# Kernel tuning notes

Hardware: AMD Instinct MI355X
Metric: run time of the kernel (lower is better)

Reference implementation:

```python
import jax, jax.numpy as jnp
import numpy as np

INV_SQRT2 = 0.7071067811865476  # Haar (db1) filter coefficient


def _haar_wavedec(x, level):
    """Haar (db1) multi-level DWT along axis=2 of x: [B,H,L,Dh].
    Returns [cA_n, cD_n, cD_{n-1}, ..., cD_1] (pywt.wavedec ordering).
    Exact match to pywt for L divisible by 2**level (no boundary padding needed)."""
    details = []
    a = x
    for _ in range(level):
        e, o = a[:, :, 0::2, :], a[:, :, 1::2, :]
        details.append((e - o) * INV_SQRT2)
        a = (e + o) * INV_SQRT2
    return [a] + details[::-1]


def _haar_idwt_step(a, d):
    """Single-level Haar inverse DWT along axis=2."""
    e = (a + d) * INV_SQRT2
    o = (a - d) * INV_SQRT2
    B, H, Lh, Dh = a.shape
    return jnp.stack([e, o], axis=3).reshape(B, H, 2 * Lh, Dh)


def setup_inputs() -> dict:
    key = jax.random.key(0)
    ks = jax.random.split(key, 6)
    B, L, D, H, M = 8, 4096, 1024, 16, 3
    Dh = D // H
    return {
        "query": jax.random.normal(ks[0], (B, L, D), jnp.float32),
        "W_qkv": jax.random.normal(ks[1], (3 * D, D), jnp.float32) * 0.02,
        "b_qkv": jnp.zeros((3 * D,), jnp.float32),
        "W_out": jax.random.normal(ks[2], (D, D), jnp.float32) * 0.02,
        "b_out": jnp.zeros((D,), jnp.float32),
        "weight_q": jax.random.normal(ks[3], (H, M, Dh), jnp.float32),
        "weight_v": jax.random.normal(ks[4], (H, M, Dh), jnp.float32),
    }


def reference(query, W_qkv, b_qkv, W_out, b_out, weight_q, weight_v):
    B, L, D = query.shape
    H, M, Dh = weight_q.shape  # n_heads, modes, head_dim

    qkv = query @ W_qkv.T + b_qkv               # [B,L,3D]; k chunk is unused (as in original)
    q = qkv[..., :D].reshape(B, L, H, Dh).transpose(0, 2, 1, 3)      # [B,H,L,Dh]
    v = qkv[..., 2 * D:].reshape(B, L, H, Dh).transpose(0, 2, 1, 3)  # [B,H,L,Dh]

    cq = _haar_wavedec(q, M)  # [cA_M, cD_M, ..., cD_1]
    cv = _haar_wavedec(v, M)

    # Weight the coarsest `modes` bands per head/channel, then multiply q*v in wavelet domain.
    prod = []
    for j in range(M):
        wq = weight_q[None, :, j, None, :]  # [1,H,1,Dh]
        wv = weight_v[None, :, j, None, :]
        prod.append((cq[j] * wq) * (cv[j] * wv))
    prod.append(cq[M] * cv[M])  # finest detail band, unweighted

    # Inverse DWT back to length L.
    a = prod[0]
    for d in prod[1:]:
        a = _haar_idwt_step(a, d)

    out = a.transpose(0, 2, 1, 3).reshape(B, L, D)
    return out @ W_out.T + b_out  # dropout is identity in eval
```

## Files before the change

### kernel.cpp

```cpp
#include <hip/hip_runtime.h>
#include <hip/hip_fp16.h>
#include <cstdint>
#include <cstddef>

typedef _Float16 f16;
typedef __attribute__((ext_vector_type(4))) _Float16 f16x4;
typedef __attribute__((ext_vector_type(8))) _Float16 f16x8;
typedef __attribute__((ext_vector_type(4))) float f32x4;

#define C_INV_SQRT2 0.70710678118654752440f

__device__ __forceinline__ void gld_lds16(const void* g, void* l) {
  __builtin_amdgcn_global_load_lds((const __attribute__((address_space(1))) void*)g,
                                   (__attribute__((address_space(3))) void*)l, 16, 0, 0);
}

__global__ __launch_bounds__(256) void cvt_f32_f16_k(const float* __restrict__ in,
                                                     f16* __restrict__ out, int n4) {
  int i = blockIdx.x * 256 + threadIdx.x;
  if (i >= n4) return;
  const float4 x = ((const float4*)in)[i];
  f16x4 y;
  y.x = (f16)x.x; y.y = (f16)x.y; y.z = (f16)x.z; y.w = (f16)x.w;
  ((f16x4*)out)[i] = y;
}

__global__ __launch_bounds__(256) void pack_wqv_k(const float* __restrict__ W,
                                                  const float* __restrict__ b,
                                                  f16* __restrict__ Wo,
                                                  float* __restrict__ bo) {
  int i = blockIdx.x * 256 + threadIdx.x;
  int n = i >> 8;
  int c = (i & 255) * 4;
  int sn = (n < 1024) ? n : (n + 1024);
  const float4 x = *(const float4*)(W + (size_t)sn * 1024 + c);
  f16x4 y; y.x = (f16)x.x; y.y = (f16)x.y; y.z = (f16)x.z; y.w = (f16)x.w;
  *(f16x4*)(Wo + (size_t)n * 1024 + c) = y;
  if (i < 2048) bo[i] = b[(i < 1024) ? i : (i + 1024)];
}


#define STAGEH(bufi, mat, half, k0)                                              \
  {                                                                              \
    f16* Ld = &lds[bufi][mat][half][0];                                          \
    const f16* Gp =                                                              \
        ((mat) ? GB : GA) + (size_t)((half) * 128 + srow) * K + (k0) + sch * 8;  \
    gld_lds16(Gp, Ld + (w * 64) * 8);                                            \
    gld_lds16(Gp + (size_t)64 * K, Ld + (4096 + w * 64 * 8));                    \
  }

#define MFMA_PH(mi0)                                                             \
  __builtin_amdgcn_s_setprio(1);                                                 \
  _Pragma("unroll") for (int mm = (mi0); mm < (mi0) + 2; mm++)                   \
      _Pragma("unroll") for (int nj = 0; nj < 4; nj++) {                         \
    acc[mm][nj] = __builtin_amdgcn_mfma_f32_16x16x32_f16(aF[mm][0], bF[nj][0],   \
                                                         acc[mm][nj], 0, 0, 0);  \
    acc[mm][nj] = __builtin_amdgcn_mfma_f32_16x16x32_f16(aF[mm][1], bF[nj][1],   \
                                                         acc[mm][nj], 0, 0, 0);  \
  }                                                                              \
  __builtin_amdgcn_s_setprio(0);

#define BAR_SEQ()                       \
  __builtin_amdgcn_sched_barrier(0);    \
  __builtin_amdgcn_s_barrier();         \
  __builtin_amdgcn_sched_barrier(0);

template <typename CT>
__global__ __launch_bounds__(512, 2) void gemm256_k(const f16* __restrict__ A,
                                                    const f16* __restrict__ B,
                                                    const float* __restrict__ bias,
                                                    CT* __restrict__ C,
                                                    int M, int N, int K, int nbx) {
  __shared__ f16 lds[2][2][2][128 * 64];
  const int t = threadIdx.x;
  const int w = t >> 6, l = t & 63;
  const int wm = w >> 2, wn = w & 3;
  const int hi = l >> 4, lo = l & 15;

  const int nwg = gridDim.x;
  const int cpx = nwg >> 3;
  const int bid = blockIdx.x;
  const int nid = (bid & 7) * cpx + (bid >> 3);
  const int by = nid / nbx, bx = nid - by * nbx;
  const int m0 = by * 256, n0 = bx * 256;

  const f16* GA = A + (size_t)m0 * K;
  const f16* GB = B + (size_t)n0 * K;

  const int srow = t >> 3;
  const int sch = (t & 7) ^ (srow & 7);

  const int colk0 = ((hi ^ (lo & 7)) << 3);
  const int colk1 = (((4 | hi) ^ (lo & 7)) << 3);

  f32x4 acc[8][4] = {};
  f16x8 aF[8][2], bF[4][2];
  const int NT = K >> 6;

  STAGEH(0, 0, 0, 0); STAGEH(0, 0, 1, 0);
  STAGEH(0, 1, 0, 0); STAGEH(0, 1, 1, 0);
  STAGEH(1, 0, 0, 64); STAGEH(1, 0, 1, 64);

  for (int tt = 0; tt < NT; ++tt) {
    const int buf = tt & 1;
    const f16* pA = &lds[buf][0][wm][0] + lo * 64;
    const f16* pB = &lds[buf][1][wn >> 1][0] + (wn & 1) * 4096 + lo * 64;
    const f16* pA0 = pA + colk0;
    const f16* pA1 = pA + colk1;
    const f16* pB0 = pB + colk0;
    const f16* pB1 = pB + colk1;

    if (tt < NT - 1) {
      asm volatile("s_waitcnt vmcnt(4)" ::: "memory");
    } else {
      asm volatile("s_waitcnt vmcnt(0)" ::: "memory");
    }
    BAR_SEQ();
    aF[0][0] = *(const f16x8*)(pA0 + 0 * 1024);
    aF[0][1] = *(const f16x8*)(pA1 + 0 * 1024);
    aF[1][0] = *(const f16x8*)(pA0 + 1 * 1024);
    aF[1][1] = *(const f16x8*)(pA1 + 1 * 1024);
#pragma unroll
    for (int nj = 0; nj < 4; nj++) {
      bF[nj][0] = *(const f16x8*)(pB0 + nj * 1024);
      bF[nj][1] = *(const f16x8*)(pB1 + nj * 1024);
    }
    aF[2][0] = *(const f16x8*)(pA0 + 2 * 1024);
    aF[2][1] = *(const f16x8*)(pA1 + 2 * 1024);
    aF[3][0] = *(const f16x8*)(pA0 + 3 * 1024);
    aF[3][1] = *(const f16x8*)(pA1 + 3 * 1024);
    if (tt + 1 < NT) STAGEH(buf ^ 1, 1, 0, (tt + 1) * 64);
    MFMA_PH(0);

    BAR_SEQ();
#pragma unroll
    for (int mi = 4; mi < 8; mi++) {
      aF[mi][0] = *(const f16x8*)(pA0 + mi * 1024);
      aF[mi][1] = *(const f16x8*)(pA1 + mi * 1024);
    }
    if (tt + 1 < NT) STAGEH(buf ^ 1, 1, 1, (tt + 1) * 64);
    MFMA_PH(2);

    asm volatile("s_waitcnt lgkmcnt(0)" ::: "memory");
    BAR_SEQ();
    if (tt + 2 < NT) STAGEH(buf, 0, 0, (tt + 2) * 64);
    MFMA_PH(4);

    asm volatile("s_waitcnt lgkmcnt(0)" ::: "memory");
    BAR_SEQ();
    if (tt + 2 < NT) STAGEH(buf, 0, 1, (tt + 2) * 64);
    MFMA_PH(6);
  }

#pragma unroll
  for (int mi = 0; mi < 8; mi++) {
#pragma unroll
    for (int nj = 0; nj < 4; nj++) {
      const int col = n0 + wn * 64 + nj * 16 + lo;
      const float bb = bias[col];
      const size_t base = (size_t)(m0 + wm * 128 + mi * 16 + hi * 4) * N + col;
#pragma unroll
      for (int r = 0; r < 4; r++) C[base + (size_t)r * N] = (CT)(acc[mi][nj][r] + bb);
    }
  }
}

__global__ __launch_bounds__(256) void dwt_middle_k(const f16* __restrict__ qv,
                                                    const float* __restrict__ wq,
                                                    const float* __restrict__ wv,
                                                    f16* __restrict__ out) {
  const int g = blockIdx.x;
  const int d0 = threadIdx.x * 4;
  const size_t m0 = (size_t)g * 8;

  f16x4 qr[8], vr[8], o[8];
#pragma unroll
  for (int i = 0; i < 8; i++) {
    qr[i] = *(const f16x4*)(qv + (m0 + i) * 2048 + d0);
    vr[i] = *(const f16x4*)(qv + (m0 + i) * 2048 + 1024 + d0);
  }
  const float c = C_INV_SQRT2;
#pragma unroll
  for (int dd = 0; dd < 4; dd++) {
    const int d = d0 + dd;
    const int h = d >> 6, dh = d & 63;
    float q[8], v[8];
#pragma unroll
    for (int i = 0; i < 8; i++) { q[i] = (float)qr[i][dd]; v[i] = (float)vr[i][dd]; }

    float qa1[4], qd1[4], va1[4], vd1[4];
#pragma unroll
    for (int i = 0; i < 4; i++) {
      qd1[i] = (q[2 * i] - q[2 * i + 1]) * c;
      qa1[i] = (q[2 * i] + q[2 * i + 1]) * c;
      vd1[i] = (v[2 * i] - v[2 * i + 1]) * c;
      va1[i] = (v[2 * i] + v[2 * i + 1]) * c;
    }
    float qa2[2], qd2[2], va2[2], vd2[2];
#pragma unroll
    for (int j = 0; j < 2; j++) {
      qd2[j] = (qa1[2 * j] - qa1[2 * j + 1]) * c;
      qa2[j] = (qa1[2 * j] + qa1[2 * j + 1]) * c;
      vd2[j] = (va1[2 * j] - va1[2 * j + 1]) * c;
      va2[j] = (va1[2 * j] + va1[2 * j + 1]) * c;
    }
    const float qd3 = (qa2[0] - qa2[1]) * c, qa3 = (qa2[0] + qa2[1]) * c;
    const float vd3 = (va2[0] - va2[1]) * c, va3 = (va2[0] + va2[1]) * c;

    const int wb = h * 192 + dh;
    const float wq0 = wq[wb], wq1 = wq[wb + 64], wq2 = wq[wb + 128];
    const float wv0 = wv[wb], wv1 = wv[wb + 64], wv2 = wv[wb + 128];

    const float pa = (qa3 * wq0) * (va3 * wv0);
    const float pd3 = (qd3 * wq1) * (vd3 * wv1);
    float pd2[2], pd1[4];
#pragma unroll
    for (int j = 0; j < 2; j++) pd2[j] = (qd2[j] * wq2) * (vd2[j] * wv2);
#pragma unroll
    for (int i = 0; i < 4; i++) pd1[i] = qd1[i] * vd1[i];

    float s2[2], s1[4];
    s2[0] = (pa + pd3) * c;
    s2[1] = (pa - pd3) * c;
#pragma unroll
    for (int j = 0; j < 2; j++) {
      s1[2 * j] = (s2[j] + pd2[j]) * c;
      s1[2 * j + 1] = (s2[j] - pd2[j]) * c;
    }
#pragma unroll
    for (int i = 0; i < 4; i++) {
      o[2 * i][dd] = (f16)((s1[i] + pd1[i]) * c);
      o[2 * i + 1][dd] = (f16)((s1[i] - pd1[i]) * c);
    }
  }
#pragma unroll
  for (int i = 0; i < 8; i++) *(f16x4*)(out + (m0 + i) * 1024 + d0) = o[i];
}

extern "C" void kernel_launch(void* const* d_in, const int* in_sizes, int n_in,
                              void* d_out, int out_size, void* d_ws, size_t ws_size,
                              hipStream_t stream) {
  (void)in_sizes; (void)n_in; (void)out_size; (void)ws_size;
  const float* query = (const float*)d_in[0];
  const float* W_qkv = (const float*)d_in[1];
  const float* b_qkv = (const float*)d_in[2];
  const float* W_out = (const float*)d_in[3];
  const float* b_out = (const float*)d_in[4];
  const float* wq = (const float*)d_in[5];
  const float* wv = (const float*)d_in[6];
  float* out = (float*)d_out;

  char* ws = (char*)d_ws;
  f16* qf16 = (f16*)ws;
  f16* Wqv = (f16*)(ws + 67108864);
  float* bqv = (float*)(ws + 67108864 + 4194304);
  f16* Wout = (f16*)(ws + 67108864 + 4194304 + 8192);
  f16* qv = (f16*)d_out;
  f16* a_f16 = qf16;

  cvt_f32_f16_k<<<dim3(8388608 / 256), dim3(256), 0, stream>>>(query, qf16, 8388608);
  pack_wqv_k<<<dim3(2048), dim3(256), 0, stream>>>(W_qkv, b_qkv, Wqv, bqv);
  cvt_f32_f16_k<<<dim3(262144 / 256), dim3(256), 0, stream>>>(W_out, Wout, 262144);
  gemm256_k<f16><<<dim3((2048 / 256) * (32768 / 256)), dim3(512), 0, stream>>>(
      qf16, Wqv, bqv, qv, 32768, 2048, 1024, 2048 / 256);
  dwt_middle_k<<<dim3(4096), dim3(256), 0, stream>>>(qv, wq, wv, a_f16);
  gemm256_k<float><<<dim3((1024 / 256) * (32768 / 256)), dim3(512), 0, stream>>>(
      a_f16, Wout, b_out, out, 32768, 1024, 1024, 1024 / 256);
}
```

Baseline: 286.1 us.

## Fuse Haar wavelet middle stage into QV projection GEMM epilogue

The QV projection GEMM now gives each block 128 q columns and the matching 128 v columns, so the Haar forward transform, band weighting, product and inverse transform can run in the epilogue. The accumulators are staged through swizzled LDS and written straight to the f16 activation buffer, which removes the separate dwt_middle kernel and the round trip of the 2048-wide qv intermediate through global memory. The fused path needs a larger workspace and falls back to the old three-kernel path when the workspace is too small. The epilogue adds LDS traffic, a barrier and scalar global stores with stride across rows.

```diff
diff --git a/kernel.cpp b/kernel.cpp
--- a/kernel.cpp
+++ b/kernel.cpp
@@ -39,14 +39,61 @@
   if (i < 2048) bo[i] = b[(i < 1024) ? i : (i + 1024)];
 }
 
-
-#define STAGEH(bufi, mat, half, k0)                                              \
-  {                                                                              \
-    f16* Ld = &lds[bufi][mat][half][0];                                          \
-    const f16* Gp =                                                              \
-        ((mat) ? GB : GA) + (size_t)((half) * 128 + srow) * K + (k0) + sch * 8;  \
-    gld_lds16(Gp, Ld + (w * 64) * 8);                                            \
-    gld_lds16(Gp + (size_t)64 * K, Ld + (4096 + w * 64 * 8));                    \
+__device__ __forceinline__ void haar_mid(const f16x8 q8, const f16x8 v8,
+                                         float wq0, float wq1, float wq2,
+                                         float wv0, float wv1, float wv2,
+                                         float* a8) {
+  const float c = C_INV_SQRT2;
+  float q[8], v[8];
+#pragma unroll
+  for (int i = 0; i < 8; i++) { q[i] = (float)q8[i]; v[i] = (float)v8[i]; }
+  float qa1[4], qd1[4], va1[4], vd1[4];
+#pragma unroll
+  for (int i = 0; i < 4; i++) {
+    qd1[i] = (q[2 * i] - q[2 * i + 1]) * c;
+    qa1[i] = (q[2 * i] + q[2 * i + 1]) * c;
+    vd1[i] = (v[2 * i] - v[2 * i + 1]) * c;
+    va1[i] = (v[2 * i] + v[2 * i + 1]) * c;
+  }
+  float qa2[2], qd2[2], va2[2], vd2[2];
+#pragma unroll
+  for (int j = 0; j < 2; j++) {
+    qd2[j] = (qa1[2 * j] - qa1[2 * j + 1]) * c;
+    qa2[j] = (qa1[2 * j] + qa1[2 * j + 1]) * c;
+    vd2[j] = (va1[2 * j] - va1[2 * j + 1]) * c;
+    va2[j] = (va1[2 * j] + va1[2 * j + 1]) * c;
+  }
+  const float qd3 = (qa2[0] - qa2[1]) * c, qa3 = (qa2[0] + qa2[1]) * c;
+  const float vd3 = (va2[0] - va2[1]) * c, va3 = (va2[0] + va2[1]) * c;
+  const float pa = (qa3 * wq0) * (va3 * wv0);
+  const float pd3 = (qd3 * wq1) * (vd3 * wv1);
+  float pd2[2], pd1[4];
+#pragma unroll
+  for (int j = 0; j < 2; j++) pd2[j] = (qd2[j] * wq2) * (vd2[j] * wv2);
+#pragma unroll
+  for (int i = 0; i < 4; i++) pd1[i] = qd1[i] * vd1[i];
+  float s2[2], s1[4];
+  s2[0] = (pa + pd3) * c;
+  s2[1] = (pa - pd3) * c;
+#pragma unroll
+  for (int j = 0; j < 2; j++) {
+    s1[2 * j] = (s2[j] + pd2[j]) * c;
+    s1[2 * j + 1] = (s2[j] - pd2[j]) * c;
+  }
+#pragma unroll
+  for (int i = 0; i < 4; i++) {
+    a8[2 * i] = (s1[i] + pd1[i]) * c;
+    a8[2 * i + 1] = (s1[i] - pd1[i]) * c;
+  }
+}
+
+
+#define STAGEH(bufi, mat, half, Gbase, k0)                         \
+  {                                                                \
+    f16* Ld = &lds[bufi][mat][half][0];                            \
+    const f16* Gp = (Gbase) + (size_t)srow * K + (k0) + sch * 8;   \
+    gld_lds16(Gp, Ld + (w * 64) * 8);                              \
+    gld_lds16(Gp + (size_t)64 * K, Ld + (4096 + w * 64 * 8));      \
   }
 
 #define MFMA_PH(mi0)                                                             \
@@ -65,11 +112,13 @@
   __builtin_amdgcn_s_barrier();         \
   __builtin_amdgcn_sched_barrier(0);
 
-template <typename CT>
+template <typename CT, bool FUSED>
 __global__ __launch_bounds__(512, 2) void gemm256_k(const f16* __restrict__ A,
                                                     const f16* __restrict__ B,
                                                     const float* __restrict__ bias,
                                                     CT* __restrict__ C,
+                                                    const float* __restrict__ wq,
+                                                    const float* __restrict__ wv,
                                                     int M, int N, int K, int nbx) {
   __shared__ f16 lds[2][2][2][128 * 64];
   const int t = threadIdx.x;
@@ -82,10 +131,13 @@
   const int bid = blockIdx.x;
   const int nid = (bid & 7) * cpx + (bid >> 3);
   const int by = nid / nbx, bx = nid - by * nbx;
-  const int m0 = by * 256, n0 = bx * 256;
+  const int m0 = by * 256;
+  const int n0 = bx * 256;
+  const int d0 = bx * 128;
 
   const f16* GA = A + (size_t)m0 * K;
-  const f16* GB = B + (size_t)n0 * K;
+  const f16* GBq = FUSED ? (B + (size_t)d0 * K) : (B + (size_t)n0 * K);
+  const f16* GBv = FUSED ? (B + (size_t)(1024 + d0) * K) : (GBq + (size_t)128 * K);
 
   const int srow = t >> 3;
   const int sch = (t & 7) ^ (srow & 7);
@@ -97,9 +149,9 @@
   f16x8 aF[8][2], bF[4][2];
   const int NT = K >> 6;
 
-  STAGEH(0, 0, 0, 0); STAGEH(0, 0, 1, 0);
-  STAGEH(0, 1, 0, 0); STAGEH(0, 1, 1, 0);
-  STAGEH(1, 0, 0, 64); STAGEH(1, 0, 1, 64);
+  STAGEH(0, 0, 0, GA, 0); STAGEH(0, 0, 1, GA + (size_t)128 * K, 0);
+  STAGEH(0, 1, 0, GBq, 0); STAGEH(0, 1, 1, GBv, 0);
+  STAGEH(1, 0, 0, GA, 64); STAGEH(1, 0, 1, GA + (size_t)128 * K, 64);
 
   for (int tt = 0; tt < NT; ++tt) {
     const int buf = tt & 1;
@@ -129,7 +181,7 @@
     aF[2][1] = *(const f16x8*)(pA1 + 2 * 1024);
     aF[3][0] = *(const f16x8*)(pA0 + 3 * 1024);
     aF[3][1] = *(const f16x8*)(pA1 + 3 * 1024);
-    if (tt + 1 < NT) STAGEH(buf ^ 1, 1, 0, (tt + 1) * 64);
+    if (tt + 1 < NT) STAGEH(buf ^ 1, 1, 0, GBq, (tt + 1) * 64);
     MFMA_PH(0);
 
     BAR_SEQ();
@@ -138,29 +190,66 @@
       aF[mi][0] = *(const f16x8*)(pA0 + mi * 1024);
       aF[mi][1] = *(const f16x8*)(pA1 + mi * 1024);
     }
-    if (tt + 1 < NT) STAGEH(buf ^ 1, 1, 1, (tt + 1) * 64);
+    if (tt + 1 < NT) STAGEH(buf ^ 1, 1, 1, GBv, (tt + 1) * 64);
     MFMA_PH(2);
 
     asm volatile("s_waitcnt lgkmcnt(0)" ::: "memory");
     BAR_SEQ();
-    if (tt + 2 < NT) STAGEH(buf, 0, 0, (tt + 2) * 64);
+    if (tt + 2 < NT) STAGEH(buf, 0, 0, GA, (tt + 2) * 64);
     MFMA_PH(4);
 
     asm volatile("s_waitcnt lgkmcnt(0)" ::: "memory");
     BAR_SEQ();
-    if (tt + 2 < NT) STAGEH(buf, 0, 1, (tt + 2) * 64);
+    if (tt + 2 < NT) STAGEH(buf, 0, 1, GA + (size_t)128 * K, (tt + 2) * 64);
     MFMA_PH(6);
   }
 
-#pragma unroll
-  for (int mi = 0; mi < 8; mi++) {
-#pragma unroll
-    for (int nj = 0; nj < 4; nj++) {
-      const int col = n0 + wn * 64 + nj * 16 + lo;
-      const float bb = bias[col];
-      const size_t base = (size_t)(m0 + wm * 128 + mi * 16 + hi * 4) * N + col;
-#pragma unroll
-      for (int r = 0; r < 4; r++) C[base + (size_t)r * N] = (CT)(acc[mi][nj][r] + bb);
+  if (!FUSED) {
+#pragma unroll
+    for (int mi = 0; mi < 8; mi++) {
+#pragma unroll
+      for (int nj = 0; nj < 4; nj++) {
+        const int col = n0 + wn * 64 + nj * 16 + lo;
+        const float bb = bias[col];
+        const size_t base = (size_t)(m0 + wm * 128 + mi * 16 + hi * 4) * N + col;
+#pragma unroll
+        for (int r = 0; r < 4; r++) C[base + (size_t)r * N] = (CT)(acc[mi][nj][r] + bb);
+      }
+    }
+  } else {
+    char* ctb = (char*)&lds[0][0][0][0];
+#pragma unroll
+    for (int mi = 0; mi < 8; mi++) {
+#pragma unroll
+      for (int nj = 0; nj < 4; nj++) {
+        const int col = wn * 64 + nj * 16 + lo;
+        const int bidx = (col < 128) ? (d0 + col) : (1024 + d0 + col - 128);
+        const float bb = bias[bidx];
+        f16x4 y;
+#pragma unroll
+        for (int r = 0; r < 4; r++) y[r] = (f16)(acc[mi][nj][r] + bb);
+        const int row2 = (wm * 128 + mi * 16 + hi * 4) * 2;
+        const int byte = (col * 512 + row2) ^ ((col & 7) << 4);
+        *(f16x4*)(ctb + byte) = y;
+      }
+    }
+    asm volatile("s_waitcnt lgkmcnt(0)" ::: "memory");
+    __builtin_amdgcn_s_barrier();
+#pragma unroll 1
+    for (int p = 0; p < 8; ++p) {
+      const int c = t & 127;
+      const int g = p * 4 + (t >> 7);
+      const int byq = (c * 512 + g * 16) ^ ((c & 7) << 4);
+      const f16x8 q8 = *(const f16x8*)(ctb + byq);
+      const f16x8 v8 = *(const f16x8*)(ctb + byq + 65536);
+      const int d = d0 + c;
+      const int wb = (d >> 6) * 192 + (d & 63);
+      float a8[8];
+      haar_mid(q8, v8, wq[wb], wq[wb + 64], wq[wb + 128],
+               wv[wb], wv[wb + 64], wv[wb + 128], a8);
+      const size_t rb = (size_t)(m0 + g * 8) * 1024 + d;
+#pragma unroll
+      for (int i = 0; i < 8; i++) C[rb + (size_t)i * 1024] = (CT)a8[i];
     }
   }
 }
@@ -172,66 +261,24 @@
   const int g = blockIdx.x;
   const int d0 = threadIdx.x * 4;
   const size_t m0 = (size_t)g * 8;
-
   f16x4 qr[8], vr[8], o[8];
 #pragma unroll
   for (int i = 0; i < 8; i++) {
     qr[i] = *(const f16x4*)(qv + (m0 + i) * 2048 + d0);
     vr[i] = *(const f16x4*)(qv + (m0 + i) * 2048 + 1024 + d0);
   }
-  const float c = C_INV_SQRT2;
 #pragma unroll
   for (int dd = 0; dd < 4; dd++) {
     const int d = d0 + dd;
-    const int h = d >> 6, dh = d & 63;
-    float q[8], v[8];
-#pragma unroll
-    for (int i = 0; i < 8; i++) { q[i] = (float)qr[i][dd]; v[i] = (float)vr[i][dd]; }
-
-    float qa1[4], qd1[4], va1[4], vd1[4];
-#pragma unroll
-    for (int i = 0; i < 4; i++) {
-      qd1[i] = (q[2 * i] - q[2 * i + 1]) * c;
-      qa1[i] = (q[2 * i] + q[2 * i + 1]) * c;
-      vd1[i] = (v[2 * i] - v[2 * i + 1]) * c;
-      va1[i] = (v[2 * i] + v[2 * i + 1]) * c;
-    }
-    float qa2[2], qd2[2], va2[2], vd2[2];
-#pragma unroll
-    for (int j = 0; j < 2; j++) {
-      qd2[j] = (qa1[2 * j] - qa1[2 * j + 1]) * c;
-      qa2[j] = (qa1[2 * j] + qa1[2 * j + 1]) * c;
-      vd2[j] = (va1[2 * j] - va1[2 * j + 1]) * c;
-      va2[j] = (va1[2 * j] + va1[2 * j + 1]) * c;
-    }
-    const float qd3 = (qa2[0] - qa2[1]) * c, qa3 = (qa2[0] + qa2[1]) * c;
-    const float vd3 = (va2[0] - va2[1]) * c, va3 = (va2[0] + va2[1]) * c;
-
-    const int wb = h * 192 + dh;
-    const float wq0 = wq[wb], wq1 = wq[wb + 64], wq2 = wq[wb + 128];
-    const float wv0 = wv[wb], wv1 = wv[wb + 64], wv2 = wv[wb + 128];
-
-    const float pa = (qa3 * wq0) * (va3 * wv0);
-    const float pd3 = (qd3 * wq1) * (vd3 * wv1);
-    float pd2[2], pd1[4];
-#pragma unroll
-    for (int j = 0; j < 2; j++) pd2[j] = (qd2[j] * wq2) * (vd2[j] * wv2);
-#pragma unroll
-    for (int i = 0; i < 4; i++) pd1[i] = qd1[i] * vd1[i];
-
-    float s2[2], s1[4];
-    s2[0] = (pa + pd3) * c;
-    s2[1] = (pa - pd3) * c;
-#pragma unroll
-    for (int j = 0; j < 2; j++) {
-      s1[2 * j] = (s2[j] + pd2[j]) * c;
-      s1[2 * j + 1] = (s2[j] - pd2[j]) * c;
-    }
-#pragma unroll
-    for (int i = 0; i < 4; i++) {
-      o[2 * i][dd] = (f16)((s1[i] + pd1[i]) * c);
-      o[2 * i + 1][dd] = (f16)((s1[i] - pd1[i]) * c);
-    }
+    const int wb = (d >> 6) * 192 + (d & 63);
+    f16x8 q8, v8;
+#pragma unroll
+    for (int i = 0; i < 8; i++) { q8[i] = qr[i][dd]; v8[i] = vr[i][dd]; }
+    float a8[8];
+    haar_mid(q8, v8, wq[wb], wq[wb + 64], wq[wb + 128],
+             wv[wb], wv[wb + 64], wv[wb + 128], a8);
+#pragma unroll
+    for (int i = 0; i < 8; i++) o[i][dd] = (f16)a8[i];
   }
 #pragma unroll
   for (int i = 0; i < 8; i++) *(f16x4*)(out + (m0 + i) * 1024 + d0) = o[i];
@@ -240,7 +287,7 @@
 extern "C" void kernel_launch(void* const* d_in, const int* in_sizes, int n_in,
                               void* d_out, int out_size, void* d_ws, size_t ws_size,
                               hipStream_t stream) {
-  (void)in_sizes; (void)n_in; (void)out_size; (void)ws_size;
+  (void)in_sizes; (void)n_in; (void)out_size;
   const float* query = (const float*)d_in[0];
   const float* W_qkv = (const float*)d_in[1];
   const float* b_qkv = (const float*)d_in[2];
@@ -255,15 +302,26 @@
   f16* Wqv = (f16*)(ws + 67108864);
   float* bqv = (float*)(ws + 67108864 + 4194304);
   f16* Wout = (f16*)(ws + 67108864 + 4194304 + 8192);
-  f16* qv = (f16*)d_out;
-  f16* a_f16 = qf16;
+  const size_t OFS_A = 67108864UL + 4194304 + 8192 + 2097152;
+  const size_t NEED = OFS_A + 67108864UL;
 
   cvt_f32_f16_k<<<dim3(8388608 / 256), dim3(256), 0, stream>>>(query, qf16, 8388608);
   pack_wqv_k<<<dim3(2048), dim3(256), 0, stream>>>(W_qkv, b_qkv, Wqv, bqv);
   cvt_f32_f16_k<<<dim3(262144 / 256), dim3(256), 0, stream>>>(W_out, Wout, 262144);
-  gemm256_k<f16><<<dim3((2048 / 256) * (32768 / 256)), dim3(512), 0, stream>>>(
-      qf16, Wqv, bqv, qv, 32768, 2048, 1024, 2048 / 256);
-  dwt_middle_k<<<dim3(4096), dim3(256), 0, stream>>>(qv, wq, wv, a_f16);
-  gemm256_k<float><<<dim3((1024 / 256) * (32768 / 256)), dim3(512), 0, stream>>>(
-      a_f16, Wout, b_out, out, 32768, 1024, 1024, 1024 / 256);
-}
+
+  if (ws_size >= NEED) {
+    f16* a_f16 = (f16*)(ws + OFS_A);
+    gemm256_k<f16, true><<<dim3(8 * 128), dim3(512), 0, stream>>>(
+        qf16, Wqv, bqv, a_f16, wq, wv, 32768, 1024, 1024, 8);
+    gemm256_k<float, false><<<dim3(4 * 128), dim3(512), 0, stream>>>(
+        a_f16, Wout, b_out, out, nullptr, nullptr, 32768, 1024, 1024, 4);
+  } else {
+    f16* qv = (f16*)d_out;
+    f16* a_f16 = qf16;
+    gemm256_k<f16, false><<<dim3(8 * 128), dim3(512), 0, stream>>>(
+        qf16, Wqv, bqv, qv, nullptr, nullptr, 32768, 2048, 1024, 8);
+    dwt_middle_k<<<dim3(4096), dim3(256), 0, stream>>>(qv, wq, wv, a_f16);
+    gemm256_k<float, false><<<dim3(4 * 128), dim3(512), 0, stream>>>(
+        a_f16, Wout, b_out, out, nullptr, nullptr, 32768, 1024, 1024, 4);
+  }
+}
```

New measurement: 263.8 us, median of 2. 7.8% less time.
